# Optimization experiments

Measured on AMD Instinct MI355X. Metric: run time of the kernel, lower is better.

## Reference

```python
import jax, jax.numpy as jnp
import numpy as np

N_NODES = 100000
N_EDGES = 6400000
N_FEAT = 128
HIDDEN = 16
OUT = 2
N_GRAPHS = 64


def setup_inputs() -> dict:
    key = jax.random.key(0)
    ks = jax.random.split(key, 8)
    x = jax.random.normal(ks[0], (N_NODES, N_FEAT), dtype=jnp.float32)
    edge_index = jax.random.randint(ks[1], (2, N_EDGES), 0, N_NODES, dtype=jnp.int64)
    batch_idx = jnp.sort(jax.random.randint(ks[2], (N_NODES,), 0, N_GRAPHS, dtype=jnp.int64))
    # GCNConv params (Glorot-ish scale)
    W1 = jax.random.normal(ks[3], (N_FEAT, HIDDEN), dtype=jnp.float32) / np.sqrt(N_FEAT)
    b1 = jnp.zeros((HIDDEN,), dtype=jnp.float32)
    prelu_a = jnp.full((1,), 0.25, dtype=jnp.float32)  # torch.nn.PReLU default
    W2 = jax.random.normal(ks[4], (HIDDEN, OUT), dtype=jnp.float32) / np.sqrt(HIDDEN)
    b2 = jnp.zeros((OUT,), dtype=jnp.float32)
    return {"x": x, "W1": W1, "b1": b1, "prelu_a": prelu_a, "W2": W2, "b2": b2,
            "edge_index": edge_index, "batch_idx": batch_idx}


def _gcn_conv(h, W, b, src, dst, norm, n_nodes):
    h = h @ W                                  # [N, d_out]
    msg = h[src] * norm[:, None]               # gather + normalize, [E', d_out]
    agg = jax.ops.segment_sum(msg, dst, num_segments=n_nodes)  # scatter-add
    return agg + b


def reference(x, W1, b1, prelu_a, W2, b2, edge_index, batch_idx):
    n_nodes = x.shape[0]
    # GCNConv default: add self-loops, symmetric normalization D^-1/2 A D^-1/2
    loops = jnp.arange(n_nodes, dtype=edge_index.dtype)
    src = jnp.concatenate([edge_index[0], loops])
    dst = jnp.concatenate([edge_index[1], loops])
    deg = jax.ops.segment_sum(jnp.ones_like(dst, dtype=x.dtype), dst, num_segments=n_nodes)
    dinv = jnp.where(deg > 0, jax.lax.rsqrt(deg), 0.0)
    norm = dinv[src] * dinv[dst]               # [E']

    h = _gcn_conv(x, W1, b1, src, dst, norm, n_nodes)
    h = jnp.where(h >= 0, h, prelu_a * h)      # PReLU (single shared slope)
    h = _gcn_conv(h, W2, b2, src, dst, norm, n_nodes)

    # global mean pool over graphs
    sums = jax.ops.segment_sum(h, batch_idx, num_segments=N_GRAPHS)
    cnts = jax.ops.segment_sum(jnp.ones((n_nodes,), dtype=h.dtype), batch_idx, num_segments=N_GRAPHS)
    return sums / jnp.maximum(cnts, 1.0)[:, None]
```

## Files before the change

kernel.cpp:

```cpp
#include <hip/hip_runtime.h>

#define NFEAT 128
#define HID 16
#define NOUT 2
#define NGRAPH 64

#define BN 196
#define NBUCK 512
#define NCB 512
#define CH 12500
#define EPT 13
#define GCNT_TOT (NBUCK * NCB)
#define SCAN_NB 256
#define PSTRIDE 192
#define WST 132
#define ACCST 17

#define S20F 1048576.0f
#define S20I 9.5367431640625e-7f
#define SPF  32768.0f
#define SPI  3.0517578125e-5f

typedef unsigned short ushortv8 __attribute__((ext_vector_type(8)));
typedef float fvec4 __attribute__((ext_vector_type(4)));

__device__ __forceinline__ int chunk_id(int bid) { return ((bid & 7) << 6) | (bid >> 3); }

__device__ __forceinline__ unsigned short f2bf(float f) {
    unsigned u = __float_as_uint(f);
    return (unsigned short)((u + 0x7FFFu + ((u >> 16) & 1u)) >> 16);
}

__device__ __forceinline__ float bf2f(unsigned short b) {
    return __uint_as_float(((unsigned)b) << 16);
}

__device__ __forceinline__ unsigned bucket_of(int d) { return (unsigned)d / (unsigned)BN; }

__global__ __launch_bounds__(1024) void k_count(const int* __restrict__ dst, int* __restrict__ gcnt, int E) {
    __shared__ int c[NBUCK];
    int t = threadIdx.x;
    int cid = chunk_id(blockIdx.x);
    for (int i = t; i < NBUCK; i += 1024) c[i] = 0;
    __syncthreads();
    int start = cid * CH;
    int end = min(E, start + CH);
    for (int e = start + t; e < end; e += 1024)
        atomicAdd(&c[bucket_of(__builtin_nontemporal_load(dst + e))], 1);
    __syncthreads();
    for (int i = t; i < NBUCK; i += 1024) gcnt[i * NCB + cid] = c[i];
}

__global__ __launch_bounds__(1024) void k_scan1(int* __restrict__ gcnt, int* __restrict__ bsum) {
    __shared__ int sh[1024];
    int t = threadIdx.x;
    int idx = blockIdx.x * 1024 + t;
    int v = (idx < GCNT_TOT) ? gcnt[idx] : 0;
    sh[t] = v;
    __syncthreads();
    for (int off = 1; off < 1024; off <<= 1) {
        int a = sh[t];
        int b = (t >= off) ? sh[t - off] : 0;
        __syncthreads();
        sh[t] = a + b;
        __syncthreads();
    }
    if (idx < GCNT_TOT) gcnt[idx] = sh[t] - v;
    if (t == 1023) bsum[blockIdx.x] = sh[1023];
}

__global__ __launch_bounds__(256) void k_scan2(int* __restrict__ bsum) {
    __shared__ int sh[256];
    int t = threadIdx.x;
    int v = (t < SCAN_NB) ? bsum[t] : 0;
    sh[t] = v;
    __syncthreads();
    for (int off = 1; off < 256; off <<= 1) {
        int a = sh[t];
        int b = (t >= off) ? sh[t - off] : 0;
        __syncthreads();
        sh[t] = a + b;
        __syncthreads();
    }
    if (t < SCAN_NB) bsum[t] = sh[t] - v;
}

__global__ __launch_bounds__(1024) void k_scan3(int* __restrict__ gcnt, const int* __restrict__ bsum) {
    int idx = blockIdx.x * 1024 + threadIdx.x;
    if (idx < GCNT_TOT) gcnt[idx] += bsum[blockIdx.x];
}

__global__ __launch_bounds__(1024) void k_scatter(const int* __restrict__ src, const int* __restrict__ dst,
                                                  const int* __restrict__ gcnt,
                                                  unsigned int* __restrict__ bpk, int E) {
    __shared__ unsigned int stage[CH + 44];
    __shared__ int hist4[4 * NBUCK];
    __shared__ int scan[512];
    __shared__ int excl[NBUCK + 1];
    __shared__ int cur[NBUCK];
    int t = threadIdx.x;
    int cid = chunk_id(blockIdx.x);
    int start = cid * CH;
    int end = min(E, start + CH);
    for (int i = t; i < 4 * NBUCK; i += 1024) hist4[i] = 0;
    __syncthreads();

    unsigned int w[EPT];
    int kb[EPT];
    int rep = (t & 3) * NBUCK;
    #pragma unroll
    for (int i = 0; i < EPT; i++) {
        int e = start + i * 1024 + t;
        kb[i] = -1;
        if (e < end) {
            int s = __builtin_nontemporal_load(src + e);
            int d = __builtin_nontemporal_load(dst + e);
            unsigned b = bucket_of(d);
            int dl = d - (int)(b * BN);
            kb[i] = (int)b;
            w[i] = ((unsigned)dl << 17) | (unsigned)s;
            atomicAdd(&hist4[rep + (int)b], 1);
        }
    }
    __syncthreads();

    int hc = 0;
    if (t < NBUCK) hc = hist4[t] + hist4[NBUCK + t] + hist4[2 * NBUCK + t] + hist4[3 * NBUCK + t];
    if (t < 512) scan[t] = (t < NBUCK) ? hc : 0;
    __syncthreads();
    for (int off = 1; off < 512; off <<= 1) {
        int a = 0;
        if (t < 512 && t >= off) a = scan[t - off];
        __syncthreads();
        if (t < 512 && t >= off) scan[t] += a;
        __syncthreads();
    }
    if (t < NBUCK) {
        int ex = scan[t] - hc;
        excl[t] = ex;
        cur[t] = ex;
    }
    if (t == 0) excl[NBUCK] = end - start;
    __syncthreads();

    #pragma unroll
    for (int i = 0; i < EPT; i++) {
        if (kb[i] >= 0) {
            int r = atomicAdd(&cur[kb[i]], 1);
            stage[r] = w[i];
        }
    }
    __syncthreads();

    int wave = t >> 6, lane = t & 63;
    for (int b = wave; b < NBUCK; b += 16) {
        int s0 = excl[b], s1 = excl[b + 1];
        int gbase = gcnt[b * NCB + cid];
        for (int j = s0 + lane; j < s1; j += 64)
            bpk[gbase + (j - s0)] = stage[j];
    }
}

__global__ __launch_bounds__(1024) void k_deg(const unsigned int* __restrict__ bpk, const int* __restrict__ gcnt,
                                              float* __restrict__ dinv, int E, int N) {
    __shared__ int h[BN];
    int t = threadIdx.x;
    int k = blockIdx.x;
    if (t < BN) h[t] = 0;
    __syncthreads();
    int bstart = gcnt[k * NCB];
    int bend = (k < NBUCK - 1) ? gcnt[(k + 1) * NCB] : E;
    for (int e = bstart + t; e < bend; e += 1024)
        atomicAdd(&h[__builtin_nontemporal_load(bpk + e) >> 17], 1);
    __syncthreads();
    if (t < BN) {
        int gn = k * BN + t;
        if (gn < N) dinv[gn] = rsqrtf(1.0f + (float)h[t]);
    }
}

__global__ __launch_bounds__(256) void k_xw1(const float* __restrict__ x, const float* __restrict__ W1,
                                             const float* __restrict__ dinv,
                                             unsigned short* __restrict__ h1b, int N) {
    __shared__ float sWT[HID * WST];
    __shared__ float sx[16 * 132];
    int t = threadIdx.x;
    for (int i = t; i < HID * NFEAT; i += 256) {
        int h = i >> 7, kk = i & 127;
        sWT[h * WST + kk] = W1[kk * HID + h];
    }
    int local = t >> 4;
    int h     = t & 15;
    int n = blockIdx.x * 16 + local;
    if (n < N) {
        const fvec4* xr = (const fvec4*)(x + (size_t)n * NFEAT);
        fvec4 a = __builtin_nontemporal_load(xr + h * 2);
        fvec4 b = __builtin_nontemporal_load(xr + h * 2 + 1);
        float* sp = sx + local * 132 + h * 8;
        ((fvec4*)sp)[0] = a;
        ((fvec4*)sp)[1] = b;
    }
    __syncthreads();
    if (n >= N) return;
    const fvec4* xr4 = (const fvec4*)(sx + local * 132);
    const fvec4* wr4 = (const fvec4*)(sWT + h * WST);
    float acc = 0.0f;
    #pragma unroll
    for (int k4 = 0; k4 < 32; k4++) {
        fvec4 a = xr4[k4];
        fvec4 b = wr4[k4];
        acc += a.x * b.x + a.y * b.y + a.z * b.z + a.w * b.w;
    }
    h1b[(size_t)n * HID + h] = f2bf(acc * dinv[n]);
}

__global__ __launch_bounds__(1024) void k_bg1(const unsigned int* __restrict__ bpk, const int* __restrict__ gcnt,
                                              const unsigned short* __restrict__ h1b, const float* __restrict__ dinv,
                                              const float* __restrict__ b1, const float* __restrict__ prelu_a,
                                              const float* __restrict__ W2,
                                              float* __restrict__ t2s, int N, int E) {
    __shared__ int acc[BN * ACCST];
    int t = threadIdx.x;
    int k = blockIdx.x;
    for (int i = t; i < BN * ACCST; i += 1024) acc[i] = 0;
    __syncthreads();
    int bstart = gcnt[k * NCB];
    int bend = (k < NBUCK - 1) ? gcnt[(k + 1) * NCB] : E;
    int q = t & 1;
    const ushortv8* h8 = (const ushortv8*)h1b;

    int e = bstart + (t >> 1);
    unsigned int w = (e < bend) ? __builtin_nontemporal_load(bpk + e) : 0u;
    while (e < bend) {
        int e2 = e + 512;
        unsigned int wn = (e2 < bend) ? __builtin_nontemporal_load(bpk + e2) : 0u;
        int d = (int)(w >> 17);
        int s = (int)(w & 0x1FFFFu);
        ushortv8 v = h8[(size_t)s * 2 + q];
        int* ap = acc + d * ACCST + q * 8;
        #pragma unroll
        for (int j = 0; j < 8; j++)
            atomicAdd(&ap[j], __float2int_rn(bf2f(v[j]) * S20F));
        w = wn;
        e = e2;
    }
    __syncthreads();

    if (t < BN * 2) {
        int n = t >> 1;
        int qq = t & 1;
        int gn = k * BN + n;
        if (gn < N) {
            float di = dinv[gn];
            float a = prelu_a[0];
            ushortv8 sv = h8[(size_t)gn * 2 + qq];
            float o0 = 0.0f, o1 = 0.0f;
            #pragma unroll
            for (int j = 0; j < 8; j++) {
                int f = qq * 8 + j;
                float tv = (float)acc[n * ACCST + f] * S20I + bf2f(sv[j]);
                tv = di * tv + b1[f];
                tv = (tv >= 0.0f) ? tv : a * tv;
                o0 += tv * W2[f * 2 + 0];
                o1 += tv * W2[f * 2 + 1];
            }
            o0 += __shfl_xor(o0, 1);
            o1 += __shfl_xor(o1, 1);
            if (qq == 0)
                *(float2*)(t2s + (size_t)gn * 2) = make_float2(di * o0, di * o1);
        }
    }
}

__global__ __launch_bounds__(1024) void k_bg2(const unsigned int* __restrict__ bpk, const int* __restrict__ gcnt,
                                              const float* __restrict__ t2s, const float* __restrict__ dinv,
                                              const int* __restrict__ batch,
                                              int* __restrict__ partials, int N, int E) {
    __shared__ int acc2[BN * 3];
    __shared__ int pg[PSTRIDE];
    int t = threadIdx.x;
    int k = blockIdx.x;
    for (int i = t; i < BN * 3; i += 1024) acc2[i] = 0;
    if (t < PSTRIDE) pg[t] = 0;
    __syncthreads();
    int bstart = gcnt[k * NCB];
    int bend = (k < NBUCK - 1) ? gcnt[(k + 1) * NCB] : E;

    int e = bstart + t;
    unsigned int w = (e < bend) ? __builtin_nontemporal_load(bpk + e) : 0u;
    while (e < bend) {
        int e2 = e + 1024;
        unsigned int wn = (e2 < bend) ? __builtin_nontemporal_load(bpk + e2) : 0u;
        int d = (int)(w >> 17);
        int s = (int)(w & 0x1FFFFu);
        float2 v = *(const float2*)(t2s + (size_t)s * 2);
        atomicAdd(&acc2[d * 3 + 0], __float2int_rn(v.x * S20F));
        atomicAdd(&acc2[d * 3 + 1], __float2int_rn(v.y * S20F));
        w = wn;
        e = e2;
    }
    __syncthreads();
    if (t < BN) {
        int gn = k * BN + t;
        if (gn < N) {
            float dd = dinv[gn];
            float2 self = *(const float2*)(t2s + (size_t)gn * 2);
            float v0 = (float)acc2[t * 3 + 0] * S20I + self.x;
            float v1 = (float)acc2[t * 3 + 1] * S20I + self.y;
            int g = batch[gn];
            atomicAdd(&pg[g * 2 + 0], __float2int_rn(dd * v0 * SPF));
            atomicAdd(&pg[g * 2 + 1], __float2int_rn(dd * v1 * SPF));
            atomicAdd(&pg[128 + g], 1);
        }
    }
    __syncthreads();
    if (t < PSTRIDE) partials[(size_t)k * PSTRIDE + t] = pg[t];
}

__global__ __launch_bounds__(256) void k_final(const int* __restrict__ partials,
                                               const float* __restrict__ b2, float* __restrict__ out) {
    __shared__ long long fsl[PSTRIDE];
    int t = threadIdx.x;
    if (t < PSTRIDE) {
        long long s0 = 0, s1 = 0, s2 = 0, s3 = 0;
        for (int r = 0; r < NBUCK; r += 4) {
            s0 += partials[(size_t)r * PSTRIDE + t];
            s1 += partials[(size_t)(r + 1) * PSTRIDE + t];
            s2 += partials[(size_t)(r + 2) * PSTRIDE + t];
            s3 += partials[(size_t)(r + 3) * PSTRIDE + t];
        }
        fsl[t] = (s0 + s1) + (s2 + s3);
    }
    __syncthreads();
    if (t < NGRAPH * NOUT) {
        int g = t >> 1, c = t & 1;
        float cnt = (float)fsl[128 + g];
        float val = (float)fsl[t] * SPI;
        out[t] = (val + cnt * b2[c]) / fmaxf(cnt, 1.0f);
    }
}

extern "C" void kernel_launch(void* const* d_in, const int* in_sizes, int n_in,
                              void* d_out, int out_size, void* d_ws, size_t ws_size,
                              hipStream_t stream) {
    const float* x       = (const float*)d_in[0];
    const float* W1      = (const float*)d_in[1];
    const float* b1      = (const float*)d_in[2];
    const float* prelu_a = (const float*)d_in[3];
    const float* W2      = (const float*)d_in[4];
    const float* b2      = (const float*)d_in[5];
    const int*   ei      = (const int*)d_in[6];
    const int*   batch   = (const int*)d_in[7];

    const int N = in_sizes[7];
    const int E = in_sizes[6] / 2;
    const int* src = ei;
    const int* dst = ei + E;

    float* ws     = (float*)d_ws;
    float* dinv   = ws;
    unsigned short* h1b = (unsigned short*)(dinv + 100352);
    float* t2s    = dinv + 100352 + (size_t)N * HID / 2;
    int*   gcnt   = (int*)(t2s + (size_t)N * NOUT);
    unsigned int* bpk = (unsigned int*)(gcnt + GCNT_TOT);
    int*   partials = (int*)(bpk + E);
    int*   bsum   = partials + (size_t)NBUCK * PSTRIDE;

    float* out = (float*)d_out;

    k_count<<<NCB, 1024, 0, stream>>>(dst, gcnt, E);
    k_scan1<<<SCAN_NB, 1024, 0, stream>>>(gcnt, bsum);
    k_scan2<<<1, 256, 0, stream>>>(bsum);
    k_scan3<<<SCAN_NB, 1024, 0, stream>>>(gcnt, bsum);
    k_scatter<<<NCB, 1024, 0, stream>>>(src, dst, gcnt, bpk, E);
    k_deg<<<NBUCK, 1024, 0, stream>>>(bpk, gcnt, dinv, E, N);
    k_xw1<<<(N + 15) / 16, 256, 0, stream>>>(x, W1, dinv, h1b, N);
    k_bg1<<<NBUCK, 1024, 0, stream>>>(bpk, gcnt, h1b, dinv, b1, prelu_a, W2, t2s, N, E);
    k_bg2<<<NBUCK, 1024, 0, stream>>>(bpk, gcnt, t2s, dinv, batch, partials, N, E);
    k_final<<<1, 256, 0, stream>>>(partials, b2, out);
}
```

Before: 286.5 us.

## Replace count+scan bucketing with fixed-capacity buckets and pack accumulators into 64-bit atomics

```diff
diff --git a/kernel.cpp b/kernel.cpp
--- a/kernel.cpp
+++ b/kernel.cpp
@@ -10,16 +10,19 @@
 #define NCB 512
 #define CH 12500
 #define EPT 13
-#define GCNT_TOT (NBUCK * NCB)
-#define SCAN_NB 256
+#define CAP 13824
 #define PSTRIDE 192
 #define WST 132
-#define ACCST 17
+#define ACST 9
 
 #define S20F 1048576.0f
 #define S20I 9.5367431640625e-7f
+#define S18F 262144.0f
+#define S18I 3.814697265625e-6f
 #define SPF  32768.0f
 #define SPI  3.0517578125e-5f
+#define OFF23 0x800000
+#define OFF22 0x400000
 
 typedef unsigned short ushortv8 __attribute__((ext_vector_type(8)));
 typedef float fvec4 __attribute__((ext_vector_type(4)));
@@ -37,61 +40,14 @@
 
 __device__ __forceinline__ unsigned bucket_of(int d) { return (unsigned)d / (unsigned)BN; }
 
-__global__ __launch_bounds__(1024) void k_count(const int* __restrict__ dst, int* __restrict__ gcnt, int E) {
-    __shared__ int c[NBUCK];
-    int t = threadIdx.x;
-    int cid = chunk_id(blockIdx.x);
-    for (int i = t; i < NBUCK; i += 1024) c[i] = 0;
-    __syncthreads();
-    int start = cid * CH;
-    int end = min(E, start + CH);
-    for (int e = start + t; e < end; e += 1024)
-        atomicAdd(&c[bucket_of(__builtin_nontemporal_load(dst + e))], 1);
-    __syncthreads();
-    for (int i = t; i < NBUCK; i += 1024) gcnt[i * NCB + cid] = c[i];
-}
-
-__global__ __launch_bounds__(1024) void k_scan1(int* __restrict__ gcnt, int* __restrict__ bsum) {
-    __shared__ int sh[1024];
-    int t = threadIdx.x;
-    int idx = blockIdx.x * 1024 + t;
-    int v = (idx < GCNT_TOT) ? gcnt[idx] : 0;
-    sh[t] = v;
-    __syncthreads();
-    for (int off = 1; off < 1024; off <<= 1) {
-        int a = sh[t];
-        int b = (t >= off) ? sh[t - off] : 0;
-        __syncthreads();
-        sh[t] = a + b;
-        __syncthreads();
-    }
-    if (idx < GCNT_TOT) gcnt[idx] = sh[t] - v;
-    if (t == 1023) bsum[blockIdx.x] = sh[1023];
-}
-
-__global__ __launch_bounds__(256) void k_scan2(int* __restrict__ bsum) {
-    __shared__ int sh[256];
-    int t = threadIdx.x;
-    int v = (t < SCAN_NB) ? bsum[t] : 0;
-    sh[t] = v;
-    __syncthreads();
-    for (int off = 1; off < 256; off <<= 1) {
-        int a = sh[t];
-        int b = (t >= off) ? sh[t - off] : 0;
-        __syncthreads();
-        sh[t] = a + b;
-        __syncthreads();
-    }
-    if (t < SCAN_NB) bsum[t] = sh[t] - v;
-}
-
-__global__ __launch_bounds__(1024) void k_scan3(int* __restrict__ gcnt, const int* __restrict__ bsum) {
-    int idx = blockIdx.x * 1024 + threadIdx.x;
-    if (idx < GCNT_TOT) gcnt[idx] += bsum[blockIdx.x];
+__global__ __launch_bounds__(1024) void k_zero(int* __restrict__ cursor, int* __restrict__ bins) {
+    int t = threadIdx.x;
+    if (t < NBUCK) cursor[t] = 0;
+    else if (t < NBUCK + 256) bins[t - NBUCK] = 0;
 }
 
 __global__ __launch_bounds__(1024) void k_scatter(const int* __restrict__ src, const int* __restrict__ dst,
-                                                  const int* __restrict__ gcnt,
+                                                  int* __restrict__ cursor,
                                                   unsigned int* __restrict__ bpk, int E) {
     __shared__ unsigned int stage[CH + 44];
     __shared__ int hist4[4 * NBUCK];
@@ -155,27 +111,35 @@
     int wave = t >> 6, lane = t & 63;
     for (int b = wave; b < NBUCK; b += 16) {
         int s0 = excl[b], s1 = excl[b + 1];
-        int gbase = gcnt[b * NCB + cid];
-        for (int j = s0 + lane; j < s1; j += 64)
-            bpk[gbase + (j - s0)] = stage[j];
-    }
-}
-
-__global__ __launch_bounds__(1024) void k_deg(const unsigned int* __restrict__ bpk, const int* __restrict__ gcnt,
-                                              float* __restrict__ dinv, int E, int N) {
+        int run = s1 - s0;
+        if (run <= 0) continue;
+        int base = 0;
+        if (lane == 0) base = atomicAdd(&cursor[b], run);
+        base = __shfl(base, 0);
+        int lim = min(run, CAP - base);
+        for (int j = lane; j < lim; j += 64)
+            bpk[(size_t)b * CAP + base + j] = stage[s0 + j];
+    }
+}
+
+__global__ __launch_bounds__(1024) void k_deg(const unsigned int* __restrict__ bpk, const int* __restrict__ cursor,
+                                              float* __restrict__ dinv, int* __restrict__ deg, int N) {
     __shared__ int h[BN];
     int t = threadIdx.x;
     int k = blockIdx.x;
     if (t < BN) h[t] = 0;
     __syncthreads();
-    int bstart = gcnt[k * NCB];
-    int bend = (k < NBUCK - 1) ? gcnt[(k + 1) * NCB] : E;
+    int bstart = k * CAP;
+    int bend = bstart + cursor[k];
     for (int e = bstart + t; e < bend; e += 1024)
         atomicAdd(&h[__builtin_nontemporal_load(bpk + e) >> 17], 1);
     __syncthreads();
     if (t < BN) {
         int gn = k * BN + t;
-        if (gn < N) dinv[gn] = rsqrtf(1.0f + (float)h[t]);
+        if (gn < N) {
+            deg[gn] = h[t];
+            dinv[gn] = rsqrtf(1.0f + (float)h[t]);
+        }
     }
 }
 
@@ -214,20 +178,21 @@
     h1b[(size_t)n * HID + h] = f2bf(acc * dinv[n]);
 }
 
-__global__ __launch_bounds__(1024) void k_bg1(const unsigned int* __restrict__ bpk, const int* __restrict__ gcnt,
+__global__ __launch_bounds__(1024) void k_bg1(const unsigned int* __restrict__ bpk, const int* __restrict__ cursor,
                                               const unsigned short* __restrict__ h1b, const float* __restrict__ dinv,
+                                              const int* __restrict__ deg,
                                               const float* __restrict__ b1, const float* __restrict__ prelu_a,
                                               const float* __restrict__ W2,
-                                              float* __restrict__ t2s, int N, int E) {
-    __shared__ int acc[BN * ACCST];
+                                              float* __restrict__ t2s, int N) {
+    __shared__ unsigned long long acc[BN * ACST];
     int t = threadIdx.x;
     int k = blockIdx.x;
-    for (int i = t; i < BN * ACCST; i += 1024) acc[i] = 0;
-    __syncthreads();
-    int bstart = gcnt[k * NCB];
-    int bend = (k < NBUCK - 1) ? gcnt[(k + 1) * NCB] : E;
+    for (int i = t; i < BN * ACST; i += 1024) acc[i] = 0ull;
+    __syncthreads();
+    int bstart = k * CAP;
+    int bend = bstart + cursor[k];
     int q = t & 1;
-    const ushortv8* h8 = (const ushortv8*)h1b;
+    const uint4* h4 = (const uint4*)h1b;
 
     int e = bstart + (t >> 1);
     unsigned int w = (e < bend) ? __builtin_nontemporal_load(bpk + e) : 0u;
@@ -236,11 +201,17 @@
         unsigned int wn = (e2 < bend) ? __builtin_nontemporal_load(bpk + e2) : 0u;
         int d = (int)(w >> 17);
         int s = (int)(w & 0x1FFFFu);
-        ushortv8 v = h8[(size_t)s * 2 + q];
-        int* ap = acc + d * ACCST + q * 8;
+        uint4 u = h4[(size_t)s * 2 + q];
+        unsigned long long* ap = acc + d * ACST + q * 4;
         #pragma unroll
-        for (int j = 0; j < 8; j++)
-            atomicAdd(&ap[j], __float2int_rn(bf2f(v[j]) * S20F));
+        for (int jj = 0; jj < 4; jj++) {
+            unsigned uu = (&u.x)[jj];
+            float flo = __uint_as_float((uu << 16) + 0x0A000000u);
+            float fhi = __uint_as_float((uu & 0xFFFF0000u) + 0x0A000000u);
+            unsigned lo = (unsigned)(__float2int_rn(flo) + OFF23);
+            unsigned hi = (unsigned)(__float2int_rn(fhi) + OFF23);
+            atomicAdd(&ap[jj], ((unsigned long long)hi << 32) | (unsigned long long)lo);
+        }
         w = wn;
         e = e2;
     }
@@ -252,17 +223,27 @@
         int gn = k * BN + n;
         if (gn < N) {
             float di = dinv[gn];
+            int dg = deg[gn];
+            long long bias = (long long)dg << 23;
             float a = prelu_a[0];
+            const ushortv8* h8 = (const ushortv8*)h1b;
             ushortv8 sv = h8[(size_t)gn * 2 + qq];
             float o0 = 0.0f, o1 = 0.0f;
             #pragma unroll
-            for (int j = 0; j < 8; j++) {
-                int f = qq * 8 + j;
-                float tv = (float)acc[n * ACCST + f] * S20I + bf2f(sv[j]);
-                tv = di * tv + b1[f];
+            for (int jj = 0; jj < 4; jj++) {
+                unsigned long long av = acc[n * ACST + qq * 4 + jj];
+                float f0 = (float)((long long)(unsigned)av - bias) * S20I;
+                float f1 = (float)((long long)(av >> 32) - bias) * S20I;
+                int fa = qq * 8 + 2 * jj;
+                float tv = di * (f0 + bf2f(sv[2 * jj])) + b1[fa];
                 tv = (tv >= 0.0f) ? tv : a * tv;
-                o0 += tv * W2[f * 2 + 0];
-                o1 += tv * W2[f * 2 + 1];
+                o0 += tv * W2[fa * 2 + 0];
+                o1 += tv * W2[fa * 2 + 1];
+                int fb = fa + 1;
+                float tw = di * (f1 + bf2f(sv[2 * jj + 1])) + b1[fb];
+                tw = (tw >= 0.0f) ? tw : a * tw;
+                o0 += tw * W2[fb * 2 + 0];
+                o1 += tw * W2[fb * 2 + 1];
             }
             o0 += __shfl_xor(o0, 1);
             o1 += __shfl_xor(o1, 1);
@@ -272,19 +253,19 @@
     }
 }
 
-__global__ __launch_bounds__(1024) void k_bg2(const unsigned int* __restrict__ bpk, const int* __restrict__ gcnt,
+__global__ __launch_bounds__(1024) void k_bg2(const unsigned int* __restrict__ bpk, const int* __restrict__ cursor,
                                               const float* __restrict__ t2s, const float* __restrict__ dinv,
-                                              const int* __restrict__ batch,
-                                              int* __restrict__ partials, int N, int E) {
-    __shared__ int acc2[BN * 3];
+                                              const int* __restrict__ deg, const int* __restrict__ batch,
+                                              int* __restrict__ bins, int N) {
+    __shared__ unsigned long long acc2[BN];
     __shared__ int pg[PSTRIDE];
     int t = threadIdx.x;
     int k = blockIdx.x;
-    for (int i = t; i < BN * 3; i += 1024) acc2[i] = 0;
+    if (t < BN) acc2[t] = 0ull;
     if (t < PSTRIDE) pg[t] = 0;
     __syncthreads();
-    int bstart = gcnt[k * NCB];
-    int bend = (k < NBUCK - 1) ? gcnt[(k + 1) * NCB] : E;
+    int bstart = k * CAP;
+    int bend = bstart + cursor[k];
 
     int e = bstart + t;
     unsigned int w = (e < bend) ? __builtin_nontemporal_load(bpk + e) : 0u;
@@ -294,8 +275,9 @@
         int d = (int)(w >> 17);
         int s = (int)(w & 0x1FFFFu);
         float2 v = *(const float2*)(t2s + (size_t)s * 2);
-        atomicAdd(&acc2[d * 3 + 0], __float2int_rn(v.x * S20F));
-        atomicAdd(&acc2[d * 3 + 1], __float2int_rn(v.y * S20F));
+        unsigned lo = (unsigned)(__float2int_rn(v.x * S18F) + OFF22);
+        unsigned hi = (unsigned)(__float2int_rn(v.y * S18F) + OFF22);
+        atomicAdd(&acc2[d], ((unsigned long long)hi << 32) | (unsigned long long)lo);
         w = wn;
         e = e2;
     }
@@ -304,9 +286,12 @@
         int gn = k * BN + t;
         if (gn < N) {
             float dd = dinv[gn];
+            int dg = deg[gn];
+            long long bias = (long long)dg << 22;
+            unsigned long long av = acc2[t];
             float2 self = *(const float2*)(t2s + (size_t)gn * 2);
-            float v0 = (float)acc2[t * 3 + 0] * S20I + self.x;
-            float v1 = (float)acc2[t * 3 + 1] * S20I + self.y;
+            float v0 = (float)((long long)(unsigned)av - bias) * S18I + self.x;
+            float v1 = (float)((long long)(av >> 32) - bias) * S18I + self.y;
             int g = batch[gn];
             atomicAdd(&pg[g * 2 + 0], __float2int_rn(dd * v0 * SPF));
             atomicAdd(&pg[g * 2 + 1], __float2int_rn(dd * v1 * SPF));
@@ -314,28 +299,16 @@
         }
     }
     __syncthreads();
-    if (t < PSTRIDE) partials[(size_t)k * PSTRIDE + t] = pg[t];
-}
-
-__global__ __launch_bounds__(256) void k_final(const int* __restrict__ partials,
+    if (t < PSTRIDE && pg[t] != 0) atomicAdd(&bins[t], pg[t]);
+}
+
+__global__ __launch_bounds__(128) void k_final(const int* __restrict__ bins,
                                                const float* __restrict__ b2, float* __restrict__ out) {
-    __shared__ long long fsl[PSTRIDE];
-    int t = threadIdx.x;
-    if (t < PSTRIDE) {
-        long long s0 = 0, s1 = 0, s2 = 0, s3 = 0;
-        for (int r = 0; r < NBUCK; r += 4) {
-            s0 += partials[(size_t)r * PSTRIDE + t];
-            s1 += partials[(size_t)(r + 1) * PSTRIDE + t];
-            s2 += partials[(size_t)(r + 2) * PSTRIDE + t];
-            s3 += partials[(size_t)(r + 3) * PSTRIDE + t];
-        }
-        fsl[t] = (s0 + s1) + (s2 + s3);
-    }
-    __syncthreads();
+    int t = threadIdx.x;
     if (t < NGRAPH * NOUT) {
         int g = t >> 1, c = t & 1;
-        float cnt = (float)fsl[128 + g];
-        float val = (float)fsl[t] * SPI;
+        float cnt = (float)bins[128 + g];
+        float val = (float)bins[t] * SPI;
         out[t] = (val + cnt * b2[c]) / fmaxf(cnt, 1.0f);
     }
 }
@@ -359,23 +332,20 @@
 
     float* ws     = (float*)d_ws;
     float* dinv   = ws;
-    unsigned short* h1b = (unsigned short*)(dinv + 100352);
-    float* t2s    = dinv + 100352 + (size_t)N * HID / 2;
-    int*   gcnt   = (int*)(t2s + (size_t)N * NOUT);
-    unsigned int* bpk = (unsigned int*)(gcnt + GCNT_TOT);
-    int*   partials = (int*)(bpk + E);
-    int*   bsum   = partials + (size_t)NBUCK * PSTRIDE;
+    int*   deg    = (int*)(dinv + 100352);
+    unsigned short* h1b = (unsigned short*)(deg + 100352);
+    float* t2s    = (float*)((int*)h1b + 802816);
+    int*   cursor = (int*)(t2s + 200064);
+    int*   bins   = cursor + 512;
+    unsigned int* bpk = (unsigned int*)(bins + 256);
 
     float* out = (float*)d_out;
 
-    k_count<<<NCB, 1024, 0, stream>>>(dst, gcnt, E);
-    k_scan1<<<SCAN_NB, 1024, 0, stream>>>(gcnt, bsum);
-    k_scan2<<<1, 256, 0, stream>>>(bsum);
-    k_scan3<<<SCAN_NB, 1024, 0, stream>>>(gcnt, bsum);
-    k_scatter<<<NCB, 1024, 0, stream>>>(src, dst, gcnt, bpk, E);
-    k_deg<<<NBUCK, 1024, 0, stream>>>(bpk, gcnt, dinv, E, N);
+    k_zero<<<1, 1024, 0, stream>>>(cursor, bins);
+    k_scatter<<<NCB, 1024, 0, stream>>>(src, dst, cursor, bpk, E);
+    k_deg<<<NBUCK, 1024, 0, stream>>>(bpk, cursor, dinv, deg, N);
     k_xw1<<<(N + 15) / 16, 256, 0, stream>>>(x, W1, dinv, h1b, N);
-    k_bg1<<<NBUCK, 1024, 0, stream>>>(bpk, gcnt, h1b, dinv, b1, prelu_a, W2, t2s, N, E);
-    k_bg2<<<NBUCK, 1024, 0, stream>>>(bpk, gcnt, t2s, dinv, batch, partials, N, E);
-    k_final<<<1, 256, 0, stream>>>(partials, b2, out);
-}
+    k_bg1<<<NBUCK, 1024, 0, stream>>>(bpk, cursor, h1b, dinv, deg, b1, prelu_a, W2, t2s, N);
+    k_bg2<<<NBUCK, 1024, 0, stream>>>(bpk, cursor, t2s, dinv, deg, batch, bins, N);
+    k_final<<<1, 128, 0, stream>>>(bins, b2, out);
+}
```

Result: slower. 787.1 us (+174.7%).
